# Performance work log

Measured on AMD Instinct MI355X. Metric: run time of the kernel, lower is better.

Reference implementation:

```python
import jax, jax.numpy as jnp
import numpy as np
from jax import lax

B, C, NH, H, W = 2, 64, 8, 256, 256
HID = int(C * 2.66)  # 170, GDFN hidden channels


def conv1x1(x, w):
    # x: [b,c,h,w], w: [o,c] (1x1 conv, no bias)
    return jnp.einsum('bchw,oc->bohw', x, w)


def dwconv3(x, w):
    # depthwise 3x3, SAME padding; w: [ch,1,3,3]
    return lax.conv_general_dilated(
        x, w, window_strides=(1, 1), padding='SAME',
        feature_group_count=x.shape[1],
        dimension_numbers=('NCHW', 'OIHW', 'NCHW'))


def ln_ch(x, w, b, eps=1e-5):
    # LayerNorm over channel dim (torch does LN on [b,hw,c] then transposes back)
    mu = jnp.mean(x, axis=1, keepdims=True)
    var = jnp.mean((x - mu) ** 2, axis=1, keepdims=True)
    return (x - mu) / jnp.sqrt(var + eps) * w[None, :, None, None] + b[None, :, None, None]


def l2norm(x, eps=1e-12):
    # F.normalize(dim=-1): x / max(||x||_2, eps)
    n = jnp.sqrt(jnp.sum(x * x, axis=-1, keepdims=True))
    return x / jnp.maximum(n, eps)


def setup_inputs() -> dict:
    key = jax.random.key(0)
    ks = jax.random.split(key, 8)
    s = 0.02
    return dict(
        x=jax.random.normal(ks[0], (B, C, H, W), jnp.float32),
        y=jax.random.normal(ks[1], (B, C, H, W), jnp.float32),
        ln11_w=jnp.ones((C,), jnp.float32), ln11_b=jnp.zeros((C,), jnp.float32),
        ln12_w=jnp.ones((C,), jnp.float32), ln12_b=jnp.zeros((C,), jnp.float32),
        ln2_w=jnp.ones((C,), jnp.float32), ln2_b=jnp.zeros((C,), jnp.float32),
        qkv_w=jax.random.normal(ks[2], (3 * C, C), jnp.float32) * s,
        qkv_dw=jax.random.normal(ks[3], (3 * C, 1, 3, 3), jnp.float32) * s,
        temperature=jnp.ones((1, NH, 1, 1), jnp.float32),
        gdfn_in_w=jax.random.normal(ks[4], (2 * HID, C), jnp.float32) * s,
        gdfn_dw=jax.random.normal(ks[5], (2 * HID, 1, 3, 3), jnp.float32) * s,
        gdfn_out_w=jax.random.normal(ks[6], (C, HID), jnp.float32) * s,
    )


def _block(x, y, ln11_w, ln11_b, ln12_w, ln12_b, ln2_w, ln2_b,
           qkv_w, qkv_dw, temperature, gdfn_in_w, gdfn_dw, gdfn_out_w):
    b, c, h, w = x.shape
    xn = ln_ch(x, ln11_w, ln11_b)
    yn = ln_ch(y, ln12_w, ln12_b)

    def qkv_heads(z):
        t = dwconv3(conv1x1(z, qkv_w), qkv_dw)
        q, k, v = jnp.split(t, 3, axis=1)
        r = lambda a: a.reshape(b, NH, c // NH, h * w)
        return r(q), r(k), r(v)

    q, k, v = qkv_heads(xn)
    q1, k1, v1 = qkv_heads(yn)
    q, k, q1, k1 = l2norm(q), l2norm(k), l2norm(q1), l2norm(k1)

    # channel attention: [b,nh,c/nh,c/nh]; only cross_feature is used by the block
    attn_du = jax.nn.softmax(jnp.einsum('bhcn,bhdn->bhcd', q1, k) * temperature, axis=-1)
    attn_ud = jax.nn.softmax(jnp.einsum('bhcn,bhdn->bhcd', q, k1) * temperature, axis=-1)
    cross = (jnp.einsum('bhcd,bhdn->bhcn', attn_du, v) +
             jnp.einsum('bhcd,bhdn->bhcn', attn_ud, v1)).reshape(b, c, h, w)

    x = x + cross

    # GDFN
    xn2 = ln_ch(x, ln2_w, ln2_b)
    t = dwconv3(conv1x1(xn2, gdfn_in_w), gdfn_dw)
    x1, x2 = jnp.split(t, 2, axis=1)
    x = x + conv1x1(jax.nn.gelu(x1, approximate=False) * x2, gdfn_out_w)
    return x


def reference(x, y, ln11_w, ln11_b, ln12_w, ln12_b, ln2_w, ln2_b,
              qkv_w, qkv_dw, temperature, gdfn_in_w, gdfn_dw, gdfn_out_w):
    return _block(x, y, ln11_w, ln11_b, ln12_w, ln12_b, ln2_w, ln2_b,
                  qkv_w, qkv_dw, temperature, gdfn_in_w, gdfn_dw, gdfn_out_w)
```

## Files before the change

### kernel.cpp

```cpp
#include <hip/hip_runtime.h>
#include <hip/hip_bf16.h>
#include <math.h>

#define HWn 65536
#define Hh 256
#define Wd 256
#define Bb 2
#define Cc 64
#define NHh 8
#define HIDc 170
#define PXN 131072

typedef __hip_bfloat16 bf16;
typedef __attribute__((ext_vector_type(8))) short short8;
typedef __attribute__((ext_vector_type(4))) short s16x4;
typedef __attribute__((ext_vector_type(4))) float f32x4;

__device__ inline float b2f(short u) {
    unsigned int x = ((unsigned int)(unsigned short)u) << 16;
    return __uint_as_float(x);
}
__device__ inline short f2b(float f) {
    __hip_bfloat16 h = __float2bfloat16(f);
    return *reinterpret_cast<short*>(&h);
}
__device__ __forceinline__ void zero8(short8& v) {
#pragma unroll
    for (int e = 0; e < 8; e++) v[e] = 0;
}

__device__ __forceinline__ void dw_row_f(const bf16* __restrict__ base, int y, int t,
                                         const float* wv, float acc[8]) {
#pragma unroll
    for (int e = 0; e < 8; e++) acc[e] = 0.f;
#pragma unroll
    for (int dy = 0; dy < 3; dy++) {
        int ys = y + dy - 1;
        if (ys < 0 || ys >= 256) continue;
        const bf16* rp = base + (size_t)ys * 2048 + (size_t)t * 8;
        short8 c8 = *reinterpret_cast<const short8*>(rp);
        short8 l8, r8;
        if (t > 0) l8 = *reinterpret_cast<const short8*>(rp - 8); else zero8(l8);
        if (t < 255) r8 = *reinterpret_cast<const short8*>(rp + 8); else zero8(r8);
#pragma unroll
        for (int e = 0; e < 8; e++)
            acc[e] += wv[e * 9 + dy * 3] * b2f(l8[e]) +
                      wv[e * 9 + dy * 3 + 1] * b2f(c8[e]) +
                      wv[e * 9 + dy * 3 + 2] * b2f(r8[e]);
    }
}

__global__ void zero_k(float* p, int n) {
    for (int i = threadIdx.x; i < n; i += 256) p[i] = 0.f;
}

__global__ __launch_bounds__(256, 2)
void ln_px(const float* __restrict__ x, const float* __restrict__ w,
           const float* __restrict__ bia, bf16* __restrict__ out) {
    int idx = blockIdx.x * 256 + threadIdx.x;
    int b = idx >> 16, p = idx & 65535;
    const float* xp = x + (size_t)b * 64 * HWn + p;
    float f[64];
    float s = 0.f;
#pragma unroll
    for (int c = 0; c < 64; c++) { f[c] = xp[(size_t)c * HWn]; s += f[c]; }
    float mu = s * (1.f / 64.f);
    float s2 = 0.f;
#pragma unroll
    for (int c = 0; c < 64; c++) { float d = f[c] - mu; s2 += d * d; }
    float inv = rsqrtf(s2 * (1.f / 64.f) + 1e-5f);
#pragma unroll
    for (int c8 = 0; c8 < 8; c8++) {
        short8 o;
#pragma unroll
        for (int e = 0; e < 8; e++) {
            int c = c8 * 8 + e;
            o[e] = f2b((f[c] - mu) * inv * w[c] + bia[c]);
        }
        *reinterpret_cast<short8*>(out + ((size_t)c8 * PXN + idx) * 8) = o;
    }
}

__global__ __launch_bounds__(256)
void conv1x1_mfma(const bf16* __restrict__ in, const float* __restrict__ w,
                  int nstrips, int remap, bf16* __restrict__ out) {
    int lane = threadIdx.x & 63, wid = threadIdx.x >> 6;
    int r16 = lane & 15, grp = lane >> 4;
    size_t px0 = (size_t)blockIdx.x * 64;
    const bf16* bp0 = in + ((size_t)grp * PXN + px0 + r16) * 8;
    const bf16* bp1 = in + (((size_t)grp + 4) * PXN + px0 + r16) * 8;
    short8 b0[4], b1[4];
#pragma unroll
    for (int s = 0; s < 4; s++) {
        b0[s] = *reinterpret_cast<const short8*>(bp0 + s * 128);
        b1[s] = *reinterpret_cast<const short8*>(bp1 + s * 128);
    }
    for (int si = wid; si < nstrips; si += 4) {
        int co = si * 16 + r16;
        int row = co;
        if (remap) row = co < 170 ? co : (co >= 176 && co < 346 ? co - 6 : -1);
        short8 a0, a1;
        if (row >= 0) {
            const float* wr = w + (size_t)row * 64 + grp * 8;
#pragma unroll
            for (int e = 0; e < 8; e++) { a0[e] = f2b(wr[e]); a1[e] = f2b(wr[32 + e]); }
        } else {
            zero8(a0); zero8(a1);
        }
        int ochunk = si * 2 + (grp >> 1);
        int osub = (grp & 1) * 4;
#pragma unroll
        for (int s = 0; s < 4; s++) {
            f32x4 acc = {0.f, 0.f, 0.f, 0.f};
            acc = __builtin_amdgcn_mfma_f32_16x16x32_bf16(a0, b0[s], acc, 0, 0, 0);
            acc = __builtin_amdgcn_mfma_f32_16x16x32_bf16(a1, b1[s], acc, 0, 0, 0);
            size_t px = px0 + s * 16 + r16;
            s16x4 o;
#pragma unroll
            for (int j = 0; j < 4; j++) o[j] = f2b(acc[j]);
            *reinterpret_cast<s16x4*>(out + ((size_t)ochunk * PXN + px) * 8 + osub) = o;
        }
    }
}

__global__ __launch_bounds__(256, 4)
void dwconv_span(const bf16* __restrict__ inx, const bf16* __restrict__ iny,
                 const float* __restrict__ w, int c0,
                 bf16* __restrict__ outx, bf16* __restrict__ outy) {
    int cid = blockIdx.x >> 7;
    int rb = blockIdx.x & 127;
    int chunk = c0 + cid;
    const bf16* in = blockIdx.y ? iny : inx;
    bf16* out = blockIdx.y ? outy : outx;
    int t = threadIdx.x;
    float wv[72];
#pragma unroll
    for (int i = 0; i < 72; i++) wv[i] = w[chunk * 72 + i];
    int b = rb >> 6;
    const bf16* base = in + ((size_t)chunk * PXN + (size_t)b * 65536) * 8;
    bf16* obase = out + ((size_t)cid * PXN + (size_t)b * 65536) * 8;
#pragma unroll
    for (int r = 0; r < 4; r++) {
        int y = (rb * 4 + r) & 255;
        float acc[8];
        dw_row_f(base, y, t, wv, acc);
        short8 o;
#pragma unroll
        for (int e = 0; e < 8; e++) o[e] = f2b(acc[e]);
        *reinterpret_cast<short8*>(obase + ((size_t)y * 256 + t) * 8) = o;
    }
}

__global__ __launch_bounds__(256, 2)
void attn_dots_px(const bf16* __restrict__ qkx, const bf16* __restrict__ qky,
                  float* __restrict__ G, float* __restrict__ NA,
                  float* __restrict__ NB) {
    int which = blockIdx.z;
    int bh = blockIdx.y;
    int b = bh >> 3, h = bh & 7;
    const bf16* Aq = (which == 0 ? qky : qkx) + ((size_t)h * PXN + (size_t)b * 65536) * 8;
    const bf16* Bk = (which == 0 ? qkx : qky) + (((size_t)8 + h) * PXN + (size_t)b * 65536) * 8;
    float acc[8][8], na[8], nb[8];
#pragma unroll
    for (int c = 0; c < 8; c++) {
        na[c] = 0.f; nb[c] = 0.f;
#pragma unroll
        for (int d = 0; d < 8; d++) acc[c][d] = 0.f;
    }
    int per = 65536 / gridDim.x;
    int n0 = blockIdx.x * per;
    for (int n = n0 + threadIdx.x; n < n0 + per; n += 256) {
        short8 q8 = *reinterpret_cast<const short8*>(Aq + (size_t)n * 8);
        short8 k8 = *reinterpret_cast<const short8*>(Bk + (size_t)n * 8);
        float av[8], bv[8];
#pragma unroll
        for (int i = 0; i < 8; i++) { av[i] = b2f(q8[i]); bv[i] = b2f(k8[i]); }
#pragma unroll
        for (int c = 0; c < 8; c++) na[c] = fmaf(av[c], av[c], na[c]);
#pragma unroll
        for (int d = 0; d < 8; d++) nb[d] = fmaf(bv[d], bv[d], nb[d]);
#pragma unroll
        for (int c = 0; c < 8; c++)
#pragma unroll
            for (int d = 0; d < 8; d++) acc[c][d] = fmaf(av[c], bv[d], acc[c][d]);
    }
    size_t gbase = (((size_t)which * Bb + b) * 8 + h);
    float* Gp = G + gbase * 64;
#pragma unroll
    for (int c = 0; c < 8; c++)
#pragma unroll
        for (int d = 0; d < 8; d++) {
            float s = acc[c][d];
#pragma unroll
            for (int m = 1; m < 64; m <<= 1) s += __shfl_xor(s, m);
            if ((threadIdx.x & 63) == 0) atomicAdd(&Gp[c * 8 + d], s);
        }
#pragma unroll
    for (int c = 0; c < 8; c++) {
        float s = na[c];
#pragma unroll
        for (int m = 1; m < 64; m <<= 1) s += __shfl_xor(s, m);
        if ((threadIdx.x & 63) == 0) atomicAdd(&NA[gbase * 8 + c], s);
        float s2 = nb[c];
#pragma unroll
        for (int m = 1; m < 64; m <<= 1) s2 += __shfl_xor(s2, m);
        if ((threadIdx.x & 63) == 0) atomicAdd(&NB[gbase * 8 + c], s2);
    }
}

__global__ void attn_softmax(const float* __restrict__ G, const float* __restrict__ NA,
                             const float* __restrict__ NB, const float* __restrict__ temp,
                             float* __restrict__ A) {
    int t = threadIdx.x;
    int h = (t >> 3) & 7;
    int c = t & 7;
    size_t rbase = t >> 3;
    const float* Gp = G + rbase * 64 + c * 8;
    float an = fmaxf(sqrtf(NA[rbase * 8 + c]), 1e-12f);
    float tm = temp[h];
    float vals[8];
    float mx = -1e30f;
#pragma unroll
    for (int d = 0; d < 8; d++) {
        float bn = fmaxf(sqrtf(NB[rbase * 8 + d]), 1e-12f);
        float v = Gp[d] / (an * bn) * tm;
        vals[d] = v;
        mx = fmaxf(mx, v);
    }
    float se = 0.f;
#pragma unroll
    for (int d = 0; d < 8; d++) { vals[d] = expf(vals[d] - mx); se += vals[d]; }
    float inv = 1.f / se;
    float* Ap = A + rbase * 64 + c * 8;
#pragma unroll
    for (int d = 0; d < 8; d++) Ap[d] = vals[d] * inv;
}

__global__ __launch_bounds__(256, 2)
void cross_ln2_px(const float* __restrict__ x, const bf16* __restrict__ vx,
                  const bf16* __restrict__ vy, const float* __restrict__ A,
                  const float* __restrict__ ln2w, const float* __restrict__ ln2b,
                  float* __restrict__ out, bf16* __restrict__ xn2) {
    int idx = blockIdx.x * 256 + threadIdx.x;
    int b = idx >> 16, p = idx & 65535;
    __shared__ float a1[512], a2[512];
    for (int i = threadIdx.x; i < 512; i += 256) {
        a1[i] = A[(size_t)b * 512 + i];
        a2[i] = A[((size_t)2 + b) * 512 + i];
    }
    __syncthreads();
    float o[64];
    const float* xp = x + (size_t)b * 64 * HWn + p;
#pragma unroll
    for (int c = 0; c < 64; c++) o[c] = xp[(size_t)c * HWn];
#pragma unroll
    for (int h = 0; h < 8; h++) {
        short8 v8 = *reinterpret_cast<const short8*>(vx + ((size_t)h * PXN + idx) * 8);
        short8 w8 = *reinterpret_cast<const short8*>(vy + ((size_t)h * PXN + idx) * 8);
        float v[8], v1[8];
#pragma unroll
        for (int d = 0; d < 8; d++) { v[d] = b2f(v8[d]); v1[d] = b2f(w8[d]); }
#pragma unroll
        for (int ci = 0; ci < 8; ci++) {
            float s = 0.f;
            const float* r1 = a1 + h * 64 + ci * 8;
            const float* r2 = a2 + h * 64 + ci * 8;
#pragma unroll
            for (int d = 0; d < 8; d++) s += r1[d] * v[d] + r2[d] * v1[d];
            o[h * 8 + ci] += s;
        }
    }
    float* op = out + (size_t)b * 64 * HWn + p;
    float s = 0.f;
#pragma unroll
    for (int c = 0; c < 64; c++) { op[(size_t)c * HWn] = o[c]; s += o[c]; }
    float mu = s * (1.f / 64.f);
    float s2 = 0.f;
#pragma unroll
    for (int c = 0; c < 64; c++) { float d = o[c] - mu; s2 += d * d; }
    float inv = rsqrtf(s2 * (1.f / 64.f) + 1e-5f);
#pragma unroll
    for (int c8 = 0; c8 < 8; c8++) {
        short8 o8;
#pragma unroll
        for (int e = 0; e < 8; e++) {
            int c = c8 * 8 + e;
            o8[e] = f2b((o[c] - mu) * inv * ln2w[c] + ln2b[c]);
        }
        *reinterpret_cast<short8*>(xn2 + ((size_t)c8 * PXN + idx) * 8) = o8;
    }
}

__global__ __launch_bounds__(256, 3)
void dwconv_gate(const bf16* __restrict__ g, const float* __restrict__ w,
                 bf16* __restrict__ tout) {
    int c = blockIdx.x >> 7;
    int rb = blockIdx.x & 127;
    int t = threadIdx.x;
    int b = rb >> 6;
    float wv[72];
#pragma unroll
    for (int i = 0; i < 72; i++)
        wv[i] = (c * 8 + i / 9 < 170) ? w[c * 72 + i] : 0.f;
    const bf16* base1 = g + ((size_t)c * PXN + (size_t)b * 65536) * 8;
    float a1r[4][8];
#pragma unroll
    for (int r = 0; r < 4; r++) {
        int y = (rb * 4 + r) & 255;
        dw_row_f(base1, y, t, wv, a1r[r]);
    }
#pragma unroll
    for (int i = 0; i < 72; i++)
        wv[i] = (c * 8 + i / 9 < 170) ? w[(170 + c * 8) * 9 + i] : 0.f;
    const bf16* base2 = g + (((size_t)22 + c) * PXN + (size_t)b * 65536) * 8;
    bf16* obase = tout + ((size_t)c * PXN + (size_t)b * 65536) * 8;
#pragma unroll
    for (int r = 0; r < 4; r++) {
        int y = (rb * 4 + r) & 255;
        float a2[8];
        dw_row_f(base2, y, t, wv, a2);
        short8 o;
#pragma unroll
        for (int e = 0; e < 8; e++) {
            float a = a1r[r][e];
            o[e] = f2b(a * 0.5f * (1.f + erff(a * 0.70710678118654752f)) * a2[e]);
        }
        *reinterpret_cast<short8*>(obase + ((size_t)y * 256 + t) * 8) = o;
    }
}

__global__ __launch_bounds__(256, 4)
void gdfn_out_mfma(const bf16* __restrict__ t, const float* __restrict__ wout,
                   float* __restrict__ out) {
    int lane = threadIdx.x & 63, wid = threadIdx.x >> 6;
    int r16 = lane & 15, grp = lane >> 4;
    size_t px0 = (size_t)blockIdx.x * 64;
    int co = wid * 16 + r16;
    short8 af[6];
#pragma unroll
    for (int kc = 0; kc < 6; kc++) {
#pragma unroll
        for (int e = 0; e < 8; e++) {
            int k = kc * 32 + grp * 8 + e;
            af[kc][e] = (k < 170) ? f2b(wout[(size_t)co * 170 + k]) : (short)0;
        }
    }
#pragma unroll
    for (int s = 0; s < 4; s++) {
        size_t px = px0 + s * 16 + r16;
        f32x4 acc = {0.f, 0.f, 0.f, 0.f};
#pragma unroll
        for (int kc = 0; kc < 6; kc++) {
            int cidx = kc * 4 + grp;
            short8 bv;
            if (cidx < 22) bv = *reinterpret_cast<const short8*>(t + ((size_t)cidx * PXN + px) * 8);
            else zero8(bv);
            acc = __builtin_amdgcn_mfma_f32_16x16x32_bf16(af[kc], bv, acc, 0, 0, 0);
        }
        int b = (int)(px >> 16);
        int p = (int)(px & 65535);
        float* op = out + (size_t)b * 64 * HWn + (size_t)(wid * 16 + grp * 4) * HWn + p;
#pragma unroll
        for (int j = 0; j < 4; j++) op[(size_t)j * HWn] += acc[j];
    }
}

extern "C" void kernel_launch(void* const* d_in, const int* in_sizes, int n_in,
                              void* d_out, int out_size, void* d_ws, size_t ws_size,
                              hipStream_t stream) {
    const float* x = (const float*)d_in[0];
    const float* y = (const float*)d_in[1];
    const float* ln11_w = (const float*)d_in[2];
    const float* ln11_b = (const float*)d_in[3];
    const float* ln12_w = (const float*)d_in[4];
    const float* ln12_b = (const float*)d_in[5];
    const float* ln2_w = (const float*)d_in[6];
    const float* ln2_b = (const float*)d_in[7];
    const float* qkv_w = (const float*)d_in[8];
    const float* qkv_dw = (const float*)d_in[9];
    const float* temp = (const float*)d_in[10];
    const float* gdfn_in_w = (const float*)d_in[11];
    const float* gdfn_dw = (const float*)d_in[12];
    const float* gdfn_out_w = (const float*)d_in[13];
    float* out = (float*)d_out;

    char* wsb = (char*)d_ws;
    float* G = (float*)wsb;
    float* NA = G + 2048;
    float* NB = NA + 256;
    float* Amat = NB + 256;
    bf16* hp = (bf16*)(wsb + 18944);
    bf16* xn   = hp;
    bf16* yn   = hp + (size_t)8388608;
    bf16* qkx  = hp;
    bf16* tx   = hp + (size_t)16777216;
    bf16* ty   = hp + (size_t)41943040;
    bf16* qky  = hp + (size_t)67108864;
    bf16* vx   = hp + (size_t)83886080;
    bf16* vy   = hp + (size_t)92274688;
    bf16* g    = hp + (size_t)16777216;
    bf16* t    = hp + (size_t)67108864;
    bf16* xn2  = hp;

    zero_k<<<1, 256, 0, stream>>>(G, 2560);

    ln_px<<<512, 256, 0, stream>>>(x, ln11_w, ln11_b, xn);
    ln_px<<<512, 256, 0, stream>>>(y, ln12_w, ln12_b, yn);

    conv1x1_mfma<<<2048, 256, 0, stream>>>(xn, qkv_w, 12, 0, tx);
    conv1x1_mfma<<<2048, 256, 0, stream>>>(yn, qkv_w, 12, 0, ty);

    dwconv_span<<<dim3(16 * 128, 2), 256, 0, stream>>>(tx, ty, qkv_dw, 0, qkx, qky);
    dwconv_span<<<dim3(8 * 128, 2), 256, 0, stream>>>(tx, ty, qkv_dw, 16, vx, vy);

    attn_dots_px<<<dim3(16, 16, 2), 256, 0, stream>>>(qkx, qky, G, NA, NB);
    attn_softmax<<<1, 256, 0, stream>>>(G, NA, NB, temp, Amat);

    cross_ln2_px<<<512, 256, 0, stream>>>(x, vx, vy, Amat, ln2_w, ln2_b, out, xn2);

    conv1x1_mfma<<<2048, 256, 0, stream>>>(xn2, gdfn_in_w, 22, 1, g);
    dwconv_gate<<<22 * 128, 256, 0, stream>>>(g, gdfn_dw, t);
    gdfn_out_mfma<<<2048, 256, 0, stream>>>(t, gdfn_out_w, out);
}
```

Baseline: 330.9 us.

## Reuse loaded rows across four output rows in depthwise convs and cheapen GELU

Depthwise 3x3 convolutions now load six input rows once and accumulate four output rows from them, instead of reloading three rows per output row. Weights are forced into scalar registers with readfirstlane, and the exact erff in the gate is replaced by an Abramowitz-Stegun polynomial approximation built on a fast reciprocal and fast exp. The gate kernel's occupancy hint is raised from 3 to 4 blocks. The erf approximation adds small error (around 1e-7 absolute), which is likely within bf16 tolerance, and holding more live rows may raise register pressure.

```diff
diff --git a/kernel.cpp b/kernel.cpp
--- a/kernel.cpp
+++ b/kernel.cpp
@@ -28,25 +28,53 @@
 #pragma unroll
     for (int e = 0; e < 8; e++) v[e] = 0;
 }
-
-__device__ __forceinline__ void dw_row_f(const bf16* __restrict__ base, int y, int t,
-                                         const float* wv, float acc[8]) {
-#pragma unroll
-    for (int e = 0; e < 8; e++) acc[e] = 0.f;
-#pragma unroll
-    for (int dy = 0; dy < 3; dy++) {
-        int ys = y + dy - 1;
-        if (ys < 0 || ys >= 256) continue;
-        const bf16* rp = base + (size_t)ys * 2048 + (size_t)t * 8;
-        short8 c8 = *reinterpret_cast<const short8*>(rp);
-        short8 l8, r8;
-        if (t > 0) l8 = *reinterpret_cast<const short8*>(rp - 8); else zero8(l8);
-        if (t < 255) r8 = *reinterpret_cast<const short8*>(rp + 8); else zero8(r8);
-#pragma unroll
-        for (int e = 0; e < 8; e++)
-            acc[e] += wv[e * 9 + dy * 3] * b2f(l8[e]) +
-                      wv[e * 9 + dy * 3 + 1] * b2f(c8[e]) +
-                      wv[e * 9 + dy * 3 + 2] * b2f(r8[e]);
+__device__ __forceinline__ float rfl(float x) {
+    return __uint_as_float(__builtin_amdgcn_readfirstlane(__float_as_uint(x)));
+}
+__device__ __forceinline__ float gelu_f(float x) {
+    float z = fabsf(x) * 0.70710678118654752f;
+    float tt = __builtin_amdgcn_rcpf(fmaf(0.3275911f, z, 1.f));
+    float p = tt * fmaf(tt, fmaf(tt, fmaf(tt, fmaf(tt, 1.061405429f, -1.453152027f),
+                                          1.421413741f), -0.284496736f), 0.254829592f);
+    float e = __expf(-z * z);
+    float er = fmaf(-p, e, 1.f);
+    er = copysignf(er, x);
+    return 0.5f * x * (1.f + er);
+}
+
+__device__ __forceinline__ void dw_load_row(const bf16* __restrict__ base, int y, int t,
+                                            float fl[8], float fc[8], float fr[8]) {
+    const bf16* rp = base + (size_t)y * 2048 + (size_t)t * 8;
+    short8 c8 = *reinterpret_cast<const short8*>(rp);
+    short8 l8, r8;
+    if (t > 0) l8 = *reinterpret_cast<const short8*>(rp - 8); else zero8(l8);
+    if (t < 255) r8 = *reinterpret_cast<const short8*>(rp + 8); else zero8(r8);
+#pragma unroll
+    for (int e = 0; e < 8; e++) { fl[e] = b2f(l8[e]); fc[e] = b2f(c8[e]); fr[e] = b2f(r8[e]); }
+}
+
+__device__ __forceinline__ void dw_quad(const bf16* __restrict__ base, int y0, int t,
+                                        const float* wv, float acc[4][8]) {
+#pragma unroll
+    for (int r = 0; r < 4; r++)
+#pragma unroll
+        for (int e = 0; e < 8; e++) acc[r][e] = 0.f;
+#pragma unroll
+    for (int j = 0; j < 6; j++) {
+        int yi = y0 - 1 + j;
+        if (yi < 0 || yi > 255) continue;
+        float fl[8], fc[8], fr[8];
+        dw_load_row(base, yi, t, fl, fc, fr);
+#pragma unroll
+        for (int r = 0; r < 4; r++) {
+            int dy = j - 1 - r;
+            if (dy < -1 || dy > 1) continue;
+            int wb = (dy + 1) * 3;
+#pragma unroll
+            for (int e = 0; e < 8; e++)
+                acc[r][e] += wv[e * 9 + wb] * fl[e] + wv[e * 9 + wb + 1] * fc[e] +
+                             wv[e * 9 + wb + 2] * fr[e];
+        }
     }
 }
 
@@ -135,19 +163,19 @@
     int t = threadIdx.x;
     float wv[72];
 #pragma unroll
-    for (int i = 0; i < 72; i++) wv[i] = w[chunk * 72 + i];
+    for (int i = 0; i < 72; i++) wv[i] = rfl(w[chunk * 72 + i]);
     int b = rb >> 6;
+    int y0 = (rb & 63) * 4;
     const bf16* base = in + ((size_t)chunk * PXN + (size_t)b * 65536) * 8;
     bf16* obase = out + ((size_t)cid * PXN + (size_t)b * 65536) * 8;
+    float acc[4][8];
+    dw_quad(base, y0, t, wv, acc);
 #pragma unroll
     for (int r = 0; r < 4; r++) {
-        int y = (rb * 4 + r) & 255;
-        float acc[8];
-        dw_row_f(base, y, t, wv, acc);
         short8 o;
 #pragma unroll
-        for (int e = 0; e < 8; e++) o[e] = f2b(acc[e]);
-        *reinterpret_cast<short8*>(obase + ((size_t)y * 256 + t) * 8) = o;
+        for (int e = 0; e < 8; e++) o[e] = f2b(acc[r][e]);
+        *reinterpret_cast<short8*>(obase + ((size_t)(y0 + r) * 256 + t) * 8) = o;
     }
 }
 
@@ -291,41 +319,35 @@
     }
 }
 
-__global__ __launch_bounds__(256, 3)
+__global__ __launch_bounds__(256, 4)
 void dwconv_gate(const bf16* __restrict__ g, const float* __restrict__ w,
                  bf16* __restrict__ tout) {
     int c = blockIdx.x >> 7;
     int rb = blockIdx.x & 127;
     int t = threadIdx.x;
     int b = rb >> 6;
+    int y0 = (rb & 63) * 4;
     float wv[72];
 #pragma unroll
     for (int i = 0; i < 72; i++)
-        wv[i] = (c * 8 + i / 9 < 170) ? w[c * 72 + i] : 0.f;
+        wv[i] = (c * 8 + i / 9 < 170) ? rfl(w[c * 72 + i]) : 0.f;
     const bf16* base1 = g + ((size_t)c * PXN + (size_t)b * 65536) * 8;
-    float a1r[4][8];
+    float a1[4][8];
+    dw_quad(base1, y0, t, wv, a1);
+#pragma unroll
+    for (int i = 0; i < 72; i++)
+        wv[i] = (c * 8 + i / 9 < 170) ? rfl(w[(170 + c * 8) * 9 + i]) : 0.f;
+    const bf16* base2 = g + (((size_t)22 + c) * PXN + (size_t)b * 65536) * 8;
+    float a2[4][8];
+    dw_quad(base2, y0, t, wv, a2);
+    bf16* obase = tout + ((size_t)c * PXN + (size_t)b * 65536) * 8;
 #pragma unroll
     for (int r = 0; r < 4; r++) {
-        int y = (rb * 4 + r) & 255;
-        dw_row_f(base1, y, t, wv, a1r[r]);
-    }
-#pragma unroll
-    for (int i = 0; i < 72; i++)
-        wv[i] = (c * 8 + i / 9 < 170) ? w[(170 + c * 8) * 9 + i] : 0.f;
-    const bf16* base2 = g + (((size_t)22 + c) * PXN + (size_t)b * 65536) * 8;
-    bf16* obase = tout + ((size_t)c * PXN + (size_t)b * 65536) * 8;
-#pragma unroll
-    for (int r = 0; r < 4; r++) {
-        int y = (rb * 4 + r) & 255;
-        float a2[8];
-        dw_row_f(base2, y, t, wv, a2);
         short8 o;
 #pragma unroll
-        for (int e = 0; e < 8; e++) {
-            float a = a1r[r][e];
-            o[e] = f2b(a * 0.5f * (1.f + erff(a * 0.70710678118654752f)) * a2[e]);
-        }
-        *reinterpret_cast<short8*>(obase + ((size_t)y * 256 + t) * 8) = o;
+        for (int e = 0; e < 8; e++)
+            o[e] = f2b(gelu_f(a1[r][e]) * a2[r][e]);
+        *reinterpret_cast<short8*>(obase + ((size_t)(y0 + r) * 256 + t) * 8) = o;
     }
 }
 
```

After: 515.1 us. 1.56x slower.
